# Optimization experiments

Hardware: AMD Instinct MI355X
Metric: run time of the kernel (lower is better)

## Reference

```python
import jax, jax.numpy as jnp
import numpy as np

BATCH = 4096
DIM = 128
TEMP = 0.5
EPS = 1e-12  # F.normalize eps


def setup_inputs() -> dict:
    key = jax.random.key(0)
    k1, k2 = jax.random.split(key)
    emb_i = jax.random.normal(k1, (BATCH, DIM), dtype=jnp.float32)
    emb_j = jax.random.normal(k2, (BATCH, DIM), dtype=jnp.float32)
    return {"emb_i": emb_i, "emb_j": emb_j}


def _l2_normalize(x):
    # matches torch.nn.functional.normalize(x, dim=1, eps=1e-12)
    n = jnp.maximum(jnp.linalg.norm(x, axis=1, keepdims=True), EPS)
    return x / n


def reference(emb_i, emb_j):
    B = BATCH
    z_i = _l2_normalize(emb_i)
    z_j = _l2_normalize(emb_j)
    reps = jnp.concatenate([z_i, z_j], axis=0)            # [2B, D]
    # cosine similarity of unit vectors == Gram matrix
    sim = reps @ reps.T                                   # [2B, 2B]
    sim_ij = jnp.diagonal(sim, offset=B)                  # [B]
    sim_ji = jnp.diagonal(sim, offset=-B)                 # [B]
    positives = jnp.concatenate([sim_ij, sim_ji], axis=0) # [2B]
    neg_mask = 1.0 - jnp.eye(2 * B, dtype=sim.dtype)
    denom = jnp.sum(neg_mask * jnp.exp(sim / TEMP), axis=1)  # [2B]
    # -log(exp(pos/T) / denom) == -pos/T + log(denom)
    loss_partial = -(positives / TEMP) + jnp.log(denom)
    loss = jnp.sum(loss_partial) / (2 * B * 5)
    return loss
```

## Files before the change

kernel.cpp:

```cpp
#include <hip/hip_runtime.h>
#include <hip/hip_bf16.h>

#define B_ROWS 4096
#define DIMN 128
#define N2 8192
#define SQRT_CEXP 1.6986436f

using f32x4 = __attribute__((ext_vector_type(4))) float;
using i32x4 = __attribute__((ext_vector_type(4))) int;
using i32x8 = __attribute__((ext_vector_type(8))) int;
typedef long i64;


__global__ __launch_bounds__(256) void normpos_k(const float* __restrict__ emb_i,
                                                 const float* __restrict__ emb_j,
                                                 i64* __restrict__ zt,
                                                 float* __restrict__ pospart) {
    const int t = threadIdx.x;
    const int lr = t >> 4;
    const int s  = t & 15;
    const int p  = blockIdx.x * 16 + lr;
    const float4* ai = (const float4*)(emb_i + (size_t)p * DIMN + s * 8);
    const float4* bj = (const float4*)(emb_j + (size_t)p * DIMN + s * 8);
    float4 a0 = ai[0], a1 = ai[1];
    float4 b0 = bj[0], b1 = bj[1];
    float sa = a0.x*a0.x + a0.y*a0.y + a0.z*a0.z + a0.w*a0.w
             + a1.x*a1.x + a1.y*a1.y + a1.z*a1.z + a1.w*a1.w;
    float sb = b0.x*b0.x + b0.y*b0.y + b0.z*b0.z + b0.w*b0.w
             + b1.x*b1.x + b1.y*b1.y + b1.z*b1.z + b1.w*b1.w;
    float dp = a0.x*b0.x + a0.y*b0.y + a0.z*b0.z + a0.w*b0.w
             + a1.x*b1.x + a1.y*b1.y + a1.z*b1.z + a1.w*b1.w;
    #pragma unroll
    for (int d = 1; d < 16; d <<= 1) {
        sa += __shfl_xor(sa, d);
        sb += __shfl_xor(sb, d);
        dp += __shfl_xor(dp, d);
    }
    float ia = __builtin_amdgcn_rsqf(fmaxf(sa, 1e-24f));
    float ib = __builtin_amdgcn_rsqf(fmaxf(sb, 1e-24f));
    float fa = ia * SQRT_CEXP, fb = ib * SQRT_CEXP;

    int wa0 = __builtin_amdgcn_cvt_pk_fp8_f32(a0.x * fa, a0.y * fa, 0, false);
    wa0     = __builtin_amdgcn_cvt_pk_fp8_f32(a0.z * fa, a0.w * fa, wa0, true);
    int wa1 = __builtin_amdgcn_cvt_pk_fp8_f32(a1.x * fa, a1.y * fa, 0, false);
    wa1     = __builtin_amdgcn_cvt_pk_fp8_f32(a1.z * fa, a1.w * fa, wa1, true);
    i64 qa = ((i64)(unsigned)wa1 << 32) | (unsigned)wa0;
    int wb0 = __builtin_amdgcn_cvt_pk_fp8_f32(b0.x * fb, b0.y * fb, 0, false);
    wb0     = __builtin_amdgcn_cvt_pk_fp8_f32(b0.z * fb, b0.w * fb, wb0, true);
    int wb1 = __builtin_amdgcn_cvt_pk_fp8_f32(b1.x * fb, b1.y * fb, 0, false);
    wb1     = __builtin_amdgcn_cvt_pk_fp8_f32(b1.z * fb, b1.w * fb, wb1, true);
    i64 qb = ((i64)(unsigned)wb1 << 32) | (unsigned)wb0;

    const int slot = ((s >> 2) * 16 + lr) * 4 + (s & 3);
    zt[(size_t)blockIdx.x * 256 + slot] = qa;
    zt[(size_t)(256 + blockIdx.x) * 256 + slot] = qb;

    __shared__ float red[16];
    if (s == 0) red[lr] = dp * ia * ib;
    __syncthreads();
    if (t == 0) {
        float x = 0.f;
        #pragma unroll
        for (int i = 0; i < 16; ++i) x += red[i];
        pospart[blockIdx.x] = x;
    }
}

template <bool MASK>
__device__ __forceinline__ void accum_step(const f32x4 (&acc)[4][2],
                                           float (&ps)[4][4],
                                           int rb, int colbase, int rq, int fr) {
    #pragma unroll
    for (int m = 0; m < 4; ++m)
        #pragma unroll
        for (int n = 0; n < 2; ++n)
            #pragma unroll
            for (int j = 0; j < 4; ++j) {
                float e = __builtin_amdgcn_exp2f(acc[m][n][j]);
                if (MASK) {
                    if (rb + m * 16 + rq + j == colbase + n * 16 + fr) e = 0.f;
                }
                ps[m][j] += e;
            }
}

__global__ __launch_bounds__(256, 3) void gram_k(const char* __restrict__ zt,
                                                 float* __restrict__ rowpart) {
    const int t = threadIdx.x;
    const int lane = t & 63;
    const int w = t >> 6;
    const int p = blockIdx.x >> 3;
    const int e = blockIdx.x & 7;
    const int rb = p * 64;
    const int fr = lane & 15;
    const int rq = (lane >> 4) * 4;

    const char* pa = zt + (size_t)(p * 4) * 2048 + lane * 32;
    const int ct0 = e * 64 + w * 16;
    const char* pb = zt + (size_t)ct0 * 2048 + lane * 32;

    i32x4 Alo[4], Ahi[4];
    #pragma unroll
    for (int m = 0; m < 4; ++m) {
        asm volatile("global_load_dwordx4 %0, %1, off"
                     : "=v"(Alo[m]) : "v"(pa + (size_t)m * 2048));
        asm volatile("global_load_dwordx4 %0, %1, off offset:16"
                     : "=v"(Ahi[m]) : "v"(pa + (size_t)m * 2048));
    }
    i32x4 Blo[2][2], Bhi[2][2];
    #pragma unroll
    for (int n = 0; n < 2; ++n) {
        asm volatile("global_load_dwordx4 %0, %1, off"
                     : "=v"(Blo[0][n]) : "v"(pb + (size_t)n * 2048));
        asm volatile("global_load_dwordx4 %0, %1, off offset:16"
                     : "=v"(Bhi[0][n]) : "v"(pb + (size_t)n * 2048));
    }
    asm volatile("s_waitcnt vmcnt(4)" ::: "memory");
    __builtin_amdgcn_sched_barrier(0);
    i32x8 A8[4];
    #pragma unroll
    for (int m = 0; m < 4; ++m)
        A8[m] = __builtin_shufflevector(Alo[m], Ahi[m], 0, 1, 2, 3, 4, 5, 6, 7);

    float ps[4][4] = {};
    #pragma unroll
    for (int s = 0; s < 8; ++s) {
        if (s < 7) {
            const char* pn = pb + (size_t)(s + 1) * 4096;
            #pragma unroll
            for (int n = 0; n < 2; ++n) {
                asm volatile("global_load_dwordx4 %0, %1, off"
                             : "=v"(Blo[(s + 1) & 1][n]) : "v"(pn + (size_t)n * 2048));
                asm volatile("global_load_dwordx4 %0, %1, off offset:16"
                             : "=v"(Bhi[(s + 1) & 1][n]) : "v"(pn + (size_t)n * 2048));
            }
            asm volatile("s_waitcnt vmcnt(4)" ::: "memory");
        } else {
            asm volatile("s_waitcnt vmcnt(0)" ::: "memory");
        }
        __builtin_amdgcn_sched_barrier(0);

        f32x4 acc[4][2] = {};
        __builtin_amdgcn_s_setprio(1);
        #pragma unroll
        for (int n = 0; n < 2; ++n) {
            i32x8 B8 = __builtin_shufflevector(Blo[s & 1][n], Bhi[s & 1][n],
                                               0, 1, 2, 3, 4, 5, 6, 7);
            #pragma unroll
            for (int m = 0; m < 4; ++m)
                acc[m][n] = __builtin_amdgcn_mfma_scale_f32_16x16x128_f8f6f4(
                    A8[m], B8, acc[m][n], 0, 0,
                    0, 0x7f7f7f7f, 0, 0x7f7f7f7f);
        }
        __builtin_amdgcn_s_setprio(0);

        const int cb = e * 1024 + w * 256 + s * 32;
        if (cb == rb || cb == rb + 32)
            accum_step<true >(acc, ps, rb, cb, rq, fr);
        else
            accum_step<false>(acc, ps, rb, cb, rq, fr);
    }

    #pragma unroll
    for (int m = 0; m < 4; ++m)
        #pragma unroll
        for (int j = 0; j < 4; ++j) {
            float v = ps[m][j];
            #pragma unroll
            for (int d = 1; d < 16; d <<= 1) v += __shfl_xor(v, d);
            ps[m][j] = v;
        }
    __shared__ float red[4][64];
    if (fr == 0) {
        #pragma unroll
        for (int m = 0; m < 4; ++m)
            #pragma unroll
            for (int j = 0; j < 4; ++j)
                red[w][m * 16 + rq + j] = ps[m][j];
    }
    __syncthreads();
    if (t < 64) {
        float ssum = red[0][t] + red[1][t] + red[2][t] + red[3][t];
        rowpart[e * N2 + rb + t] = ssum;
    }
}

__global__ void finalize_k(const float* __restrict__ rowpart,
                           const float* __restrict__ pospart,
                           float* __restrict__ out) {
    const int t = threadIdx.x;
    float acc = 0.f;
    for (int r = t; r < N2; r += 1024) {
        float d = 0.f;
        #pragma unroll
        for (int k = 0; k < 8; ++k) d += rowpart[k * N2 + r];
        acc += __builtin_amdgcn_logf(d);
    }
    acc *= 0.6931471805599453f;
    if (t < 256) acc -= 4.0f * pospart[t];
    #pragma unroll
    for (int m = 32; m; m >>= 1) acc += __shfl_xor(acc, m);
    __shared__ float red[16];
    if ((t & 63) == 0) red[t >> 6] = acc;
    __syncthreads();
    if (t == 0) {
        float x = 0.f;
        #pragma unroll
        for (int i = 0; i < 16; ++i) x += red[i];
        out[0] = x / (float)(2 * B_ROWS * 5);
    }
}

extern "C" void kernel_launch(void* const* d_in, const int* in_sizes, int n_in,
                              void* d_out, int out_size, void* d_ws, size_t ws_size,
                              hipStream_t stream) {
    const float* emb_i = (const float*)d_in[0];
    const float* emb_j = (const float*)d_in[1];
    i64* zt        = (i64*)d_ws;
    float* rowpart = (float*)((char*)d_ws + (size_t)N2 * DIMN);
    float* pospart = rowpart + 8 * N2;

    normpos_k<<<256, 256, 0, stream>>>(emb_i, emb_j, zt, pospart);
    gram_k<<<1024, 256, 0, stream>>>((const char*)zt, rowpart);
    finalize_k<<<1, 1024, 0, stream>>>(rowpart, pospart, (float*)d_out);
}
```

Measured before the change: 29.69 us.

## Fuse finalize into gram kernel via last-block atomic counter reduction

Drops the separate single-block finalize kernel. Each row-block's eight column-partition blocks bump an atomic counter, and the last one to arrive sums the row partials, takes the log, subtracts the positives and atomically adds its share into the output. The counters and the output are zeroed in the normalize kernel. This removes one kernel launch and a serial tail, at the cost of a threadfence and an atomic in every gram block, plus a nondeterministic float atomic summation order.

```diff
diff --git a/kernel.cpp b/kernel.cpp
--- a/kernel.cpp
+++ b/kernel.cpp
@@ -15,8 +15,14 @@
 __global__ __launch_bounds__(256) void normpos_k(const float* __restrict__ emb_i,
                                                  const float* __restrict__ emb_j,
                                                  i64* __restrict__ zt,
-                                                 float* __restrict__ pospart) {
+                                                 float* __restrict__ pospart,
+                                                 int* __restrict__ cnt,
+                                                 float* __restrict__ out) {
     const int t = threadIdx.x;
+    if (blockIdx.x == 0) {
+        if (t < 128) cnt[t] = 0;
+        if (t == 128) out[0] = 0.f;
+    }
     const int lr = t >> 4;
     const int s  = t & 15;
     const int p  = blockIdx.x * 16 + lr;
@@ -85,7 +91,10 @@
 }
 
 __global__ __launch_bounds__(256, 3) void gram_k(const char* __restrict__ zt,
-                                                 float* __restrict__ rowpart) {
+                                                 float* __restrict__ rowpart,
+                                                 const float* __restrict__ pospart,
+                                                 int* __restrict__ cnt,
+                                                 float* __restrict__ out) {
     const int t = threadIdx.x;
     const int lane = t & 63;
     const int w = t >> 6;
@@ -179,35 +188,32 @@
                 red[w][m * 16 + rq + j] = ps[m][j];
     }
     __syncthreads();
-    if (t < 64) {
-        float ssum = red[0][t] + red[1][t] + red[2][t] + red[3][t];
-        rowpart[e * N2 + rb + t] = ssum;
-    }
-}
-
-__global__ void finalize_k(const float* __restrict__ rowpart,
-                           const float* __restrict__ pospart,
-                           float* __restrict__ out) {
-    const int t = threadIdx.x;
-    float acc = 0.f;
-    for (int r = t; r < N2; r += 1024) {
-        float d = 0.f;
-        #pragma unroll
-        for (int k = 0; k < 8; ++k) d += rowpart[k * N2 + r];
-        acc += __builtin_amdgcn_logf(d);
-    }
-    acc *= 0.6931471805599453f;
-    if (t < 256) acc -= 4.0f * pospart[t];
-    #pragma unroll
-    for (int m = 32; m; m >>= 1) acc += __shfl_xor(acc, m);
-    __shared__ float red[16];
-    if ((t & 63) == 0) red[t >> 6] = acc;
-    __syncthreads();
-    if (t == 0) {
-        float x = 0.f;
-        #pragma unroll
-        for (int i = 0; i < 16; ++i) x += red[i];
-        out[0] = x / (float)(2 * B_ROWS * 5);
+    if (t < 64)
+        rowpart[e * N2 + rb + t] = red[0][t] + red[1][t] + red[2][t] + red[3][t];
+
+    __threadfence();
+    __syncthreads();
+    __shared__ int lastflag;
+    if (t == 0)
+        lastflag = (__hip_atomic_fetch_add(&cnt[p], 1, __ATOMIC_ACQ_REL,
+                                           __HIP_MEMORY_SCOPE_AGENT) == 7);
+    __syncthreads();
+    if (lastflag && t < 64) {
+        float dsum = 0.f;
+        #pragma unroll
+        for (int k = 0; k < 8; ++k)
+            dsum += __hip_atomic_load(&rowpart[k * N2 + rb + t],
+                                      __ATOMIC_RELAXED, __HIP_MEMORY_SCOPE_AGENT);
+        float lg = __builtin_amdgcn_logf(dsum);
+        #pragma unroll
+        for (int d = 1; d < 64; d <<= 1) lg += __shfl_xor(lg, d);
+        if (t == 0) {
+            float contrib = lg * 0.6931471805599453f;
+            if (p < 64)
+                contrib -= 4.0f * (pospart[4 * p] + pospart[4 * p + 1] +
+                                   pospart[4 * p + 2] + pospart[4 * p + 3]);
+            atomicAdd(out, contrib * (1.0f / (2.0f * B_ROWS * 5.0f)));
+        }
     }
 }
 
@@ -219,8 +225,8 @@
     i64* zt        = (i64*)d_ws;
     float* rowpart = (float*)((char*)d_ws + (size_t)N2 * DIMN);
     float* pospart = rowpart + 8 * N2;
-
-    normpos_k<<<256, 256, 0, stream>>>(emb_i, emb_j, zt, pospart);
-    gram_k<<<1024, 256, 0, stream>>>((const char*)zt, rowpart);
-    finalize_k<<<1, 1024, 0, stream>>>(rowpart, pospart, (float*)d_out);
-}
+    int*   cnt     = (int*)(pospart + 256);
+
+    normpos_k<<<256, 256, 0, stream>>>(emb_i, emb_j, zt, pospart, cnt, (float*)d_out);
+    gram_k<<<1024, 256, 0, stream>>>((const char*)zt, rowpart, pospart, cnt, (float*)d_out);
+}
```

Measured after the change: 104.1 us. 3.51x slower.

## Narrow gram B-tile to one 16-col block per step and parallelize finalize

Applied to the files above, without the earlier changes.

The gram kernel now handles one 16-column B block per iteration over 16 steps instead of two blocks over 8 steps. This halves the accumulator and B-register footprint, and the min-blocks-per-SM launch bound is dropped, presumably to reduce register pressure and shorten the exp tail per step. The finalize kernel is split across 8 blocks that atomically add into the output, which is zeroed by the first kernel. The trade is fewer MFMAs between waits, more loop iterations, and nondeterministic float summation order.

```diff
diff --git a/kernel.cpp b/kernel.cpp
--- a/kernel.cpp
+++ b/kernel.cpp
@@ -15,8 +15,10 @@
 __global__ __launch_bounds__(256) void normpos_k(const float* __restrict__ emb_i,
                                                  const float* __restrict__ emb_j,
                                                  i64* __restrict__ zt,
-                                                 float* __restrict__ pospart) {
+                                                 float* __restrict__ pospart,
+                                                 float* __restrict__ out) {
     const int t = threadIdx.x;
+    if (blockIdx.x == 0 && t == 0) out[0] = 0.f;
     const int lr = t >> 4;
     const int s  = t & 15;
     const int p  = blockIdx.x * 16 + lr;
@@ -67,25 +69,23 @@
 }
 
 template <bool MASK>
-__device__ __forceinline__ void accum_step(const f32x4 (&acc)[4][2],
+__device__ __forceinline__ void accum_step(const f32x4 (&acc)[4],
                                            float (&ps)[4][4],
-                                           int rb, int colbase, int rq, int fr) {
+                                           int rb, int cb, int rq, int fr) {
     #pragma unroll
     for (int m = 0; m < 4; ++m)
         #pragma unroll
-        for (int n = 0; n < 2; ++n)
-            #pragma unroll
-            for (int j = 0; j < 4; ++j) {
-                float e = __builtin_amdgcn_exp2f(acc[m][n][j]);
-                if (MASK) {
-                    if (rb + m * 16 + rq + j == colbase + n * 16 + fr) e = 0.f;
-                }
-                ps[m][j] += e;
+        for (int j = 0; j < 4; ++j) {
+            float e = __builtin_amdgcn_exp2f(acc[m][j]);
+            if (MASK) {
+                if (rb + m * 16 + rq + j == cb + fr) e = 0.f;
             }
-}
-
-__global__ __launch_bounds__(256, 3) void gram_k(const char* __restrict__ zt,
-                                                 float* __restrict__ rowpart) {
+            ps[m][j] += e;
+        }
+}
+
+__global__ __launch_bounds__(256) void gram_k(const char* __restrict__ zt,
+                                              float* __restrict__ rowpart) {
     const int t = threadIdx.x;
     const int lane = t & 63;
     const int w = t >> 6;
@@ -96,8 +96,7 @@
     const int rq = (lane >> 4) * 4;
 
     const char* pa = zt + (size_t)(p * 4) * 2048 + lane * 32;
-    const int ct0 = e * 64 + w * 16;
-    const char* pb = zt + (size_t)ct0 * 2048 + lane * 32;
+    const char* pb = zt + (size_t)(e * 64 + w * 16) * 2048 + lane * 32;
 
     i32x4 Alo[4], Ahi[4];
     #pragma unroll
@@ -107,15 +106,10 @@
         asm volatile("global_load_dwordx4 %0, %1, off offset:16"
                      : "=v"(Ahi[m]) : "v"(pa + (size_t)m * 2048));
     }
-    i32x4 Blo[2][2], Bhi[2][2];
-    #pragma unroll
-    for (int n = 0; n < 2; ++n) {
-        asm volatile("global_load_dwordx4 %0, %1, off"
-                     : "=v"(Blo[0][n]) : "v"(pb + (size_t)n * 2048));
-        asm volatile("global_load_dwordx4 %0, %1, off offset:16"
-                     : "=v"(Bhi[0][n]) : "v"(pb + (size_t)n * 2048));
-    }
-    asm volatile("s_waitcnt vmcnt(4)" ::: "memory");
+    i32x4 Bl[2], Bh[2];
+    asm volatile("global_load_dwordx4 %0, %1, off"           : "=v"(Bl[0]) : "v"(pb));
+    asm volatile("global_load_dwordx4 %0, %1, off offset:16" : "=v"(Bh[0]) : "v"(pb));
+    asm volatile("s_waitcnt vmcnt(2)" ::: "memory");
     __builtin_amdgcn_sched_barrier(0);
     i32x8 A8[4];
     #pragma unroll
@@ -124,41 +118,33 @@
 
     float ps[4][4] = {};
     #pragma unroll
-    for (int s = 0; s < 8; ++s) {
-        if (s < 7) {
-            const char* pn = pb + (size_t)(s + 1) * 4096;
-            #pragma unroll
-            for (int n = 0; n < 2; ++n) {
-                asm volatile("global_load_dwordx4 %0, %1, off"
-                             : "=v"(Blo[(s + 1) & 1][n]) : "v"(pn + (size_t)n * 2048));
-                asm volatile("global_load_dwordx4 %0, %1, off offset:16"
-                             : "=v"(Bhi[(s + 1) & 1][n]) : "v"(pn + (size_t)n * 2048));
-            }
-            asm volatile("s_waitcnt vmcnt(4)" ::: "memory");
+    for (int s = 0; s < 16; ++s) {
+        if (s < 15) {
+            const char* pn = pb + (size_t)(s + 1) * 2048;
+            asm volatile("global_load_dwordx4 %0, %1, off"
+                         : "=v"(Bl[(s + 1) & 1]) : "v"(pn));
+            asm volatile("global_load_dwordx4 %0, %1, off offset:16"
+                         : "=v"(Bh[(s + 1) & 1]) : "v"(pn));
+            asm volatile("s_waitcnt vmcnt(2)" ::: "memory");
         } else {
             asm volatile("s_waitcnt vmcnt(0)" ::: "memory");
         }
         __builtin_amdgcn_sched_barrier(0);
 
-        f32x4 acc[4][2] = {};
+        i32x8 B8 = __builtin_shufflevector(Bl[s & 1], Bh[s & 1],
+                                           0, 1, 2, 3, 4, 5, 6, 7);
+        f32x4 acc[4] = {};
         __builtin_amdgcn_s_setprio(1);
         #pragma unroll
-        for (int n = 0; n < 2; ++n) {
-            i32x8 B8 = __builtin_shufflevector(Blo[s & 1][n], Bhi[s & 1][n],
-                                               0, 1, 2, 3, 4, 5, 6, 7);
-            #pragma unroll
-            for (int m = 0; m < 4; ++m)
-                acc[m][n] = __builtin_amdgcn_mfma_scale_f32_16x16x128_f8f6f4(
-                    A8[m], B8, acc[m][n], 0, 0,
-                    0, 0x7f7f7f7f, 0, 0x7f7f7f7f);
-        }
+        for (int m = 0; m < 4; ++m)
+            acc[m] = __builtin_amdgcn_mfma_scale_f32_16x16x128_f8f6f4(
+                A8[m], B8, acc[m], 0, 0,
+                0, 0x7f7f7f7f, 0, 0x7f7f7f7f);
         __builtin_amdgcn_s_setprio(0);
 
-        const int cb = e * 1024 + w * 256 + s * 32;
-        if (cb == rb || cb == rb + 32)
-            accum_step<true >(acc, ps, rb, cb, rq, fr);
-        else
-            accum_step<false>(acc, ps, rb, cb, rq, fr);
+        const int cb = (e * 64 + w * 16 + s) * 16;
+        if (cb >= rb && cb < rb + 64) accum_step<true >(acc, ps, rb, cb, rq, fr);
+        else                          accum_step<false>(acc, ps, rb, cb, rq, fr);
     }
 
     #pragma unroll
@@ -179,25 +165,20 @@
                 red[w][m * 16 + rq + j] = ps[m][j];
     }
     __syncthreads();
-    if (t < 64) {
-        float ssum = red[0][t] + red[1][t] + red[2][t] + red[3][t];
-        rowpart[e * N2 + rb + t] = ssum;
-    }
+    if (t < 64)
+        rowpart[e * N2 + rb + t] = red[0][t] + red[1][t] + red[2][t] + red[3][t];
 }
 
 __global__ void finalize_k(const float* __restrict__ rowpart,
                            const float* __restrict__ pospart,
                            float* __restrict__ out) {
     const int t = threadIdx.x;
-    float acc = 0.f;
-    for (int r = t; r < N2; r += 1024) {
-        float d = 0.f;
-        #pragma unroll
-        for (int k = 0; k < 8; ++k) d += rowpart[k * N2 + r];
-        acc += __builtin_amdgcn_logf(d);
-    }
-    acc *= 0.6931471805599453f;
-    if (t < 256) acc -= 4.0f * pospart[t];
+    const int r = blockIdx.x * 1024 + t;
+    float d = 0.f;
+    #pragma unroll
+    for (int k = 0; k < 8; ++k) d += rowpart[k * N2 + r];
+    float acc = __builtin_amdgcn_logf(d) * 0.6931471805599453f;
+    if (blockIdx.x == 0 && t < 256) acc -= 4.0f * pospart[t];
     #pragma unroll
     for (int m = 32; m; m >>= 1) acc += __shfl_xor(acc, m);
     __shared__ float red[16];
@@ -207,7 +188,7 @@
         float x = 0.f;
         #pragma unroll
         for (int i = 0; i < 16; ++i) x += red[i];
-        out[0] = x / (float)(2 * B_ROWS * 5);
+        atomicAdd(out, x * (1.0f / (2.0f * B_ROWS * 5.0f)));
     }
 }
 
@@ -220,7 +201,7 @@
     float* rowpart = (float*)((char*)d_ws + (size_t)N2 * DIMN);
     float* pospart = rowpart + 8 * N2;
 
-    normpos_k<<<256, 256, 0, stream>>>(emb_i, emb_j, zt, pospart);
+    normpos_k<<<256, 256, 0, stream>>>(emb_i, emb_j, zt, pospart, (float*)d_out);
     gram_k<<<1024, 256, 0, stream>>>((const char*)zt, rowpart);
-    finalize_k<<<1, 1024, 0, stream>>>(rowpart, pospart, (float*)d_out);
-}
+    finalize_k<<<8, 1024, 0, stream>>>(rowpart, pospart, (float*)d_out);
+}
```

Measured after the change: 35.88 us. 1.21x slower.
